# Optimization experiments

Hardware: AMD Instinct MI355X
Metric: run time of the kernel (lower is better)

Reference implementation:

```python
import jax, jax.numpy as jnp
import numpy as np

N, E, G, F, H, L, NH, HD = 40000, 640000, 256, 9, 128, 3, 4, 32
EPS = 1e-5

def _ln(x, g, b):
    m = jnp.mean(x, axis=-1, keepdims=True)
    v = jnp.mean((x - m) ** 2, axis=-1, keepdims=True)
    return (x - m) * jax.lax.rsqrt(v + EPS) * g + b

def _forward(floats, edge_index, batch):
    (x, pos, emb_w, emb_b, edge_w1, edge_b1, edge_w2, edge_b2,
     node_w1, node_b1, node_w2, node_b2, qkv_w, qkv_b, out_w, out_b,
     ln1_g, ln1_b, ln2_g, ln2_b, ff_w1, ff_b1, ff_w2, ff_b2,
     cls_w1, cls_b1, cls_w2, cls_b2) = floats
    src, dst = edge_index[0], edge_index[1]  # PyG: x_j = x[src], x_i = x[dst], aggregate at dst
    dist = jnp.linalg.norm(pos[dst] - pos[src], axis=-1, keepdims=True)  # [E,1]
    h = x @ emb_w + emb_b  # [N,H]
    for l in range(L):
        # message: edge_mlp(cat[x_i, x_j, dist])
        ef = jnp.concatenate([h[dst], h[src], dist], axis=-1)  # [E,2H+1]
        m = jax.nn.silu(ef @ edge_w1[l] + edge_b1[l])
        m = jax.nn.silu(m @ edge_w2[l] + edge_b2[l])  # [E,H]
        aggr = jax.ops.segment_sum(m, dst, num_segments=N)  # [N,H]
        u = jax.nn.silu(jnp.concatenate([h, aggr], axis=-1) @ node_w1[l] + node_b1[l])
        u = u @ node_w2[l] + node_b2[l]
        h = h + u  # residual in GAHT.forward
    # per-graph mean pooling (faithful to masked-mean loop)
    sums = jax.ops.segment_sum(h, batch, num_segments=G)  # [G,H]
    cnts = jax.ops.segment_sum(jnp.ones((N,), h.dtype), batch, num_segments=G)
    g = sums / jnp.maximum(cnts, 1.0)[:, None]  # [G,H]
    # 2-layer post-norm transformer encoder (batch=1, seq=G), relu FFN, eval mode (no dropout)
    scale = 1.0 / jnp.sqrt(jnp.asarray(HD, g.dtype))
    for t in range(2):
        qkv = g @ qkv_w[t] + qkv_b[t]  # [G,3H]
        q, k, v = jnp.split(qkv, 3, axis=-1)
        q = q.reshape(G, NH, HD); k = k.reshape(G, NH, HD); v = v.reshape(G, NH, HD)
        att = jax.nn.softmax(jnp.einsum('qhd,khd->hqk', q, k) * scale, axis=-1)
        o = jnp.einsum('hqk,khd->qhd', att, v).reshape(G, H)
        o = o @ out_w[t] + out_b[t]
        g = _ln(g + o, ln1_g[t], ln1_b[t])
        ff = jax.nn.relu(g @ ff_w1[t] + ff_b1[t]) @ ff_w2[t] + ff_b2[t]
        g = _ln(g + ff, ln2_g[t], ln2_b[t])
    out = jax.nn.relu(g @ cls_w1 + cls_b1) @ cls_w2 + cls_b2  # [G,1]
    return out.squeeze(-1)  # [G]


def setup_inputs() -> dict:
    key = jax.random.key(0)
    ks = jax.random.split(key, 16)
    def p(k, shape, scale=0.08):
        return jax.random.normal(k, shape, dtype=jnp.float32) * scale
    return {
        'x': jax.random.normal(ks[0], (N, F), dtype=jnp.float32),
        'pos': jax.random.normal(ks[1], (N, 3), dtype=jnp.float32),
        'emb_w': p(ks[2], (F, H)), 'emb_b': jnp.zeros((H,), jnp.float32),
        'edge_w1': p(ks[3], (L, 2 * H + 1, H)), 'edge_b1': jnp.zeros((L, H), jnp.float32),
        'edge_w2': p(ks[4], (L, H, H)), 'edge_b2': jnp.zeros((L, H), jnp.float32),
        'node_w1': p(ks[5], (L, 2 * H, H)), 'node_b1': jnp.zeros((L, H), jnp.float32),
        'node_w2': p(ks[6], (L, H, H)), 'node_b2': jnp.zeros((L, H), jnp.float32),
        'qkv_w': p(ks[7], (2, H, 3 * H)), 'qkv_b': jnp.zeros((2, 3 * H), jnp.float32),
        'out_w': p(ks[8], (2, H, H)), 'out_b': jnp.zeros((2, H), jnp.float32),
        'ln1_g': jnp.ones((2, H), jnp.float32), 'ln1_b': jnp.zeros((2, H), jnp.float32),
        'ln2_g': jnp.ones((2, H), jnp.float32), 'ln2_b': jnp.zeros((2, H), jnp.float32),
        'ff_w1': p(ks[9], (2, H, 2 * H)), 'ff_b1': jnp.zeros((2, 2 * H), jnp.float32),
        'ff_w2': p(ks[10], (2, 2 * H, H)), 'ff_b2': jnp.zeros((2, H), jnp.float32),
        'cls_w1': p(ks[11], (H, H // 2)), 'cls_b1': jnp.zeros((H // 2,), jnp.float32),
        'cls_w2': p(ks[12], (H // 2, 1)), 'cls_b2': jnp.zeros((1,), jnp.float32),
        'edge_index': jax.random.randint(ks[13], (2, E), 0, N),
        'batch': jnp.sort(jax.random.randint(ks[14], (N,), 0, G)),
    }


def reference(x, pos, emb_w, emb_b, edge_w1, edge_b1, edge_w2, edge_b2,
              node_w1, node_b1, node_w2, node_b2, qkv_w, qkv_b, out_w, out_b,
              ln1_g, ln1_b, ln2_g, ln2_b, ff_w1, ff_b1, ff_w2, ff_b2,
              cls_w1, cls_b1, cls_w2, cls_b2, edge_index, batch):
    floats = (x, pos, emb_w, emb_b, edge_w1, edge_b1, edge_w2, edge_b2,
              node_w1, node_b1, node_w2, node_b2, qkv_w, qkv_b, out_w, out_b,
              ln1_g, ln1_b, ln2_g, ln2_b, ff_w1, ff_b1, ff_w2, ff_b2,
              cls_w1, cls_b1, cls_w2, cls_b2)
    return _forward(floats, edge_index, batch)
```

## Files before the change

kernel.cpp:

```cpp
#include <hip/hip_runtime.h>
#include <hip/hip_bf16.h>
#include <stdint.h>

#define NN 40000
#define EE 640000
#define GG 256
#define FFE 9
#define HH 128

typedef __bf16 bf16;
typedef __bf16 bf16x8 __attribute__((ext_vector_type(8)));
typedef float f32x4 __attribute__((ext_vector_type(4)));

__device__ __forceinline__ f32x4 mfma16(bf16x8 a, bf16x8 b, f32x4 c){
  return __builtin_amdgcn_mfma_f32_16x16x32_bf16(a, b, c, 0, 0, 0);
}
__device__ __forceinline__ float silu_f(float x){
  return x * __builtin_amdgcn_rcpf(1.0f + __expf(-x));
}
__device__ __forceinline__ uint16_t bfb(float x){ bf16 h=(bf16)x; return *(uint16_t*)&h; }
__device__ __forceinline__ int swz(int row, int cb){
  return row*256 + (cb ^ ((row & 7) << 4));
}

__global__ __launch_bounds__(256) void k_prep(
    const float* __restrict__ edge_w1, const float* __restrict__ edge_w2,
    const float* __restrict__ node_w1, const float* __restrict__ node_w2,
    const float* __restrict__ edge_b1,
    const float* __restrict__ x, const float* __restrict__ emb_w,
    const float* __restrict__ emb_b,
    bf16* __restrict__ wcatT, bf16* __restrict__ w2T,
    bf16* __restrict__ nw1T, bf16* __restrict__ nw2T,
    float* __restrict__ bcat, float* __restrict__ h, bf16* __restrict__ h_bf,
    int* __restrict__ cnt)
{
  int b = blockIdx.x, tid = threadIdx.x;
  if (b < 192){
    int l = b/64; int t2 = (b%64)*256 + tid;
    int n = t2 >> 7, k = t2 & 127;
    wcatT[(size_t)l*32768 + n*128 + k] = (bf16)edge_w1[(size_t)l*32896 + k*128 + n];
  } else if (b < 384){
    int lb = b - 192; int l = lb/64; int t2 = (lb%64)*256 + tid;
    int n = t2 >> 7, k = t2 & 127;
    wcatT[(size_t)l*32768 + 16384 + n*128 + k] = (bf16)edge_w1[(size_t)l*32896 + (128+k)*128 + n];
  } else if (b < 576){
    int lb = b - 384; int l = lb/64; int t2 = (lb%64)*256 + tid;
    int n = t2 >> 7, k = t2 & 127;
    w2T[(size_t)l*16384 + n*128 + k] = (bf16)edge_w2[(size_t)l*16384 + k*128 + n];
  } else if (b < 960){
    int lb = b - 576; int l = lb/128; int t2 = (lb%128)*256 + tid;
    int n = t2 >> 8, k = t2 & 255;
    nw1T[(size_t)l*32768 + n*256 + k] = (bf16)node_w1[(size_t)l*32768 + k*128 + n];
  } else if (b < 1152){
    int lb = b - 960; int l = lb/64; int t2 = (lb%64)*256 + tid;
    int n = t2 >> 7, k = t2 & 127;
    nw2T[(size_t)l*16384 + n*128 + k] = (bf16)node_w2[(size_t)l*16384 + k*128 + n];
  } else if (b < 1155){
    int l = b - 1152;
    bcat[l*256 + tid] = (tid < 128) ? edge_b1[l*128 + tid] : 0.0f;
  } else if (b < 1312){
    int i = (b - 1155)*256 + tid;
    if (i < NN) cnt[i] = 0;
  } else {
    int idx = (b - 1312)*256 + tid;
    int n = idx >> 7, f = idx & 127;
    float s = emb_b[f];
    const float* xr = x + n*FFE;
    #pragma unroll
    for (int k=0;k<FFE;++k) s += xr[k]*emb_w[k*HH + f];
    h[idx] = s;
    h_bf[idx] = (bf16)s;
  }
}

__global__ __launch_bounds__(256) void k_hist(const int* __restrict__ dst, int* __restrict__ cnt){
  int e = blockIdx.x*256 + threadIdx.x;
  if (e < EE) atomicAdd(&cnt[dst[e]], 1);
}

__global__ __launch_bounds__(1024) void k_scan(const int* __restrict__ cnt, int* __restrict__ cursor, int n){
  __shared__ int s_wsum[16];
  __shared__ int s_run;
  int tid = threadIdx.x, lane = tid & 63, wv = tid >> 6;
  if (tid == 0) s_run = 0;
  __syncthreads();
  for (int base=0; base<n; base+=4096){
    int i = base + tid*4;
    int c0 = (i  <n)? cnt[i  ] : 0;
    int c1 = (i+1<n)? cnt[i+1] : 0;
    int c2 = (i+2<n)? cnt[i+2] : 0;
    int c3 = (i+3<n)? cnt[i+3] : 0;
    int t0 = c0, t1 = t0+c1, t2 = t1+c2, t3 = t2+c3;
    int xx = t3;
    #pragma unroll
    for (int off=1; off<64; off<<=1){ int t = __shfl_up(xx, off); if (lane>=off) xx += t; }
    if (lane==63) s_wsum[wv] = xx;
    __syncthreads();
    if (wv==0 && lane<16){
      int y = s_wsum[lane];
      #pragma unroll
      for (int off=1; off<16; off<<=1){ int t = __shfl_up(y, off, 16); if (lane>=off) y += t; }
      s_wsum[lane] = y;
    }
    __syncthreads();
    int woff = wv ? s_wsum[wv-1] : 0;
    int run = s_run;
    int eb = run + woff + xx - t3;
    if (i  <n) cursor[i  ] = eb;
    if (i+1<n) cursor[i+1] = eb + t0;
    if (i+2<n) cursor[i+2] = eb + t1;
    if (i+3<n) cursor[i+3] = eb + t2;
    __syncthreads();
    if (tid==0) s_run = run + s_wsum[15];
    __syncthreads();
  }
}

__global__ __launch_bounds__(256) void k_scatter(
    const int* __restrict__ ei, const float* __restrict__ pos,
    int* __restrict__ cursor, int4* __restrict__ rec)
{
  int e = blockIdx.x*256 + threadIdx.x;
  if (e >= EE) return;
  int s = ei[e], d = ei[EE + e];
  int p = atomicAdd(&cursor[d], 1);
  float dx = pos[d*3+0]-pos[s*3+0];
  float dy = pos[d*3+1]-pos[s*3+1];
  float dz = pos[d*3+2]-pos[s*3+2];
  int4 rc; rc.x = s; rc.y = d; rc.z = __float_as_int(sqrtf(dx*dx+dy*dy+dz*dz)); rc.w = 0;
  rec[p] = rc;
}

template<int KTOT, int K1, int ACT, bool A1BF, bool BIAS, bool RESID, bool OBF, bool OF, bool ZAGGR>
__global__ __launch_bounds__(256) void k_gemm(
    const void* __restrict__ a1v, const float* __restrict__ a2,
    const bf16* __restrict__ wt, const float* __restrict__ bias,
    const float* __restrict__ resid, bf16* __restrict__ outb,
    float* __restrict__ outf, int Nw, float* __restrict__ aggr)
{
  constexpr int LDK = 136;
  __shared__ bf16 s_a[128*LDK];
  __shared__ bf16 s_w[64*LDK];
  int tid = threadIdx.x, lane = tid & 63, w = tid >> 6;
  int m0 = blockIdx.x*128, n0 = blockIdx.y*64;
  if (ZAGGR && blockIdx.y == 0){
    int nrows = NN - m0; if (nrows > 128) nrows = 128;
    f32x4 z = {0.f,0.f,0.f,0.f};
    for (int i = tid; i < nrows*32; i += 256)
      *(f32x4*)(aggr + (size_t)m0*128 + (size_t)i*4) = z;
  }
  f32x4 acc[2][4];
  #pragma unroll
  for (int i=0;i<2;++i)
    #pragma unroll
    for (int j=0;j<4;++j)
      #pragma unroll
      for (int r=0;r<4;++r) acc[i][j][r]=0.f;
  int rsel = lane & 15, ksel = (lane>>4)*8;
  int wm = w*32;

  for (int kh=0; kh<KTOT; kh+=128){
    #pragma unroll
    for (int it=0; it<8; ++it){
      int idx = tid + it*256;
      int row = idx >> 4, col = (idx & 15)*8;
      int gc = kh + col;
      int grow = m0 + row; if (grow > NN-1) grow = NN-1;
      bf16x8 vv;
      if (gc < K1){
        if (A1BF){
          vv = *(const bf16x8*)((const bf16*)a1v + (size_t)grow*K1 + gc);
        } else {
          const float* srcp = (const float*)a1v + (size_t)grow*K1 + gc;
          f32x4 u0 = *(const f32x4*)srcp;
          f32x4 u1 = *(const f32x4*)(srcp+4);
          vv[0]=(bf16)u0[0]; vv[1]=(bf16)u0[1]; vv[2]=(bf16)u0[2]; vv[3]=(bf16)u0[3];
          vv[4]=(bf16)u1[0]; vv[5]=(bf16)u1[1]; vv[6]=(bf16)u1[2]; vv[7]=(bf16)u1[3];
        }
      } else {
        const float* srcp = a2 + (size_t)grow*(KTOT-K1) + (gc-K1);
        f32x4 u0 = *(const f32x4*)srcp;
        f32x4 u1 = *(const f32x4*)(srcp+4);
        vv[0]=(bf16)u0[0]; vv[1]=(bf16)u0[1]; vv[2]=(bf16)u0[2]; vv[3]=(bf16)u0[3];
        vv[4]=(bf16)u1[0]; vv[5]=(bf16)u1[1]; vv[6]=(bf16)u1[2]; vv[7]=(bf16)u1[3];
      }
      *(bf16x8*)&s_a[row*LDK + col] = vv;
    }
    #pragma unroll
    for (int it=0; it<4; ++it){
      int idx = tid + it*256;
      int row = idx >> 4, col = (idx & 15)*8;
      *(bf16x8*)&s_w[row*LDK + col] = *(const bf16x8*)(wt + (size_t)(n0+row)*KTOT + kh + col);
    }
    __syncthreads();
    #pragma unroll
    for (int ks=0; ks<4; ++ks){
      int kb = ks*32 + ksel;
      bf16x8 fa0 = *(const bf16x8*)&s_a[(wm+rsel)*LDK + kb];
      bf16x8 fa1 = *(const bf16x8*)&s_a[(wm+16+rsel)*LDK + kb];
      #pragma unroll
      for (int j=0;j<4;++j){
        bf16x8 fb = *(const bf16x8*)&s_w[(j*16+rsel)*LDK + kb];
        acc[0][j]=mfma16(fa0,fb,acc[0][j]);
        acc[1][j]=mfma16(fa1,fb,acc[1][j]);
      }
    }
    __syncthreads();
  }

  #pragma unroll
  for (int i=0;i<2;++i){
    #pragma unroll
    for (int j=0;j<4;++j){
      int col = n0 + j*16 + rsel;
      float bv = BIAS ? bias[col] : 0.0f;
      #pragma unroll
      for (int r=0;r<4;++r){
        int row = m0 + wm + i*16 + 4*(lane>>4) + r;
        if (row < NN){
          float v = acc[i][j][r] + bv;
          if (ACT==1) v = silu_f(v);
          if (RESID) v += resid[(size_t)row*Nw + col];
          if (OBF) outb[(size_t)row*Nw + col] = (bf16)v;
          if (OF)  outf[(size_t)row*Nw + col] = v;
        }
      }
    }
  }
}

__global__ __launch_bounds__(512, 6) void k_edge(
    const bf16* __restrict__ P, const bf16* __restrict__ w2t,
    const float* __restrict__ w1r, const float* __restrict__ b2,
    const int4* __restrict__ rec, float* __restrict__ aggr)
{
  __shared__ char smem[32768];
  __shared__ int s_dst[128];
  __shared__ unsigned s_segidw[32];
  __shared__ int s_segdst[128];
  __shared__ int s_misc[4];
  int tid = threadIdx.x, lane = tid & 63, w = tid >> 6;
  int rsel = lane & 15, hi = lane >> 4;
  int bid = blockIdx.x;
  int swb = (bid & 7) * (EE/128/8) + (bid >> 3);
  int e0 = swb * 128;
  int col = w*16 + rsel;

  bf16x8 fb[4];
  #pragma unroll
  for (int ks=0;ks<4;++ks)
    fb[ks] = *(const bf16x8*)(w2t + (size_t)col*128 + ks*32 + hi*8);

  if (tid == 0){
    s_misc[0] = (e0 == 0) ? -2147483647 : rec[e0-1].y;
    s_misc[1] = (e0 + 128 >= EE) ? -2147483647 : rec[e0+128].y;
  }

  int cq = (tid & 15)*8;
  int er = tid >> 5;
  er = tid >> 4;
  int4 rc[4];
  #pragma unroll
  for (int it=0; it<4; ++it) rc[it] = rec[e0 + er + it*32];
  uint4 pau[4], pbu[4];
  #pragma unroll
  for (int it=0; it<4; ++it){
    pau[it] = *(const uint4*)(P + ((size_t)rc[it].y << 8) + cq);
    pbu[it] = *(const uint4*)(P + ((size_t)rc[it].x << 8) + 128 + cq);
  }
  if (cq == 0){
    #pragma unroll
    for (int it=0; it<4; ++it) s_dst[er + it*32] = rc[it].y;
  }
  f32x4 wr0 = *(const f32x4*)(w1r + cq);
  f32x4 wr1 = *(const f32x4*)(w1r + cq + 4);
  #pragma unroll
  for (int it=0; it<4; ++it){
    float dist = __int_as_float(rc[it].z);
    bf16x8 mm;
    #pragma unroll
    for (int j=0;j<4;++j){
      unsigned ua = ((const unsigned*)&pau[it])[j];
      unsigned ub = ((const unsigned*)&pbu[it])[j];
      float al = __uint_as_float(ua << 16);
      float ah = __uint_as_float(ua & 0xFFFF0000u);
      float bl = __uint_as_float(ub << 16);
      float bh = __uint_as_float(ub & 0xFFFF0000u);
      float wlo = (j<2) ? wr0[2*j]   : wr1[2*(j-2)];
      float whi = (j<2) ? wr0[2*j+1] : wr1[2*(j-2)+1];
      mm[2*j]   = (bf16)silu_f(al + bl + dist*wlo);
      mm[2*j+1] = (bf16)silu_f(ah + bh + dist*whi);
    }
    *(bf16x8*)(smem + swz(er + it*32, cq*2)) = mm;
  }
  __syncthreads();

  if (w == 0){
    int d0 = s_dst[2*lane], d1 = s_dst[2*lane+1];
    int dm1 = (lane == 0) ? 0 : s_dst[2*lane-1];
    int h0 = (lane == 0) ? 1 : (d0 != dm1);
    int h1 = (d1 != d0);
    int p = h0 + h1, x = p;
    #pragma unroll
    for (int off=1; off<64; off<<=1){ int t = __shfl_up(x, off); if (lane>=off) x += t; }
    int excl = x - p;
    int id0 = excl + h0 - 1;
    int id1 = excl + p - 1;
    uint8_t* sb = (uint8_t*)s_segidw;
    sb[2*lane]   = (uint8_t)id0;
    sb[2*lane+1] = (uint8_t)id1;
    if (h0) s_segdst[id0] = d0;
    if (h1) s_segdst[id1] = d1;
    if (lane == 63) s_misc[2] = id1 + 1;
  }

  f32x4 acc[8];
  #pragma unroll
  for (int mt=0;mt<8;++mt)
    #pragma unroll
    for (int r=0;r<4;++r) acc[mt][r]=0.f;
  #pragma unroll
  for (int mt=0;mt<8;++mt){
    #pragma unroll
    for (int ks=0;ks<4;++ks){
      bf16x8 fa = *(const bf16x8*)(smem + swz(mt*16 + rsel, ks*64 + hi*16));
      acc[mt] = mfma16(fa, fb[ks], acc[mt]);
    }
  }
  __syncthreads();

  float bb = b2[col];
  #pragma unroll
  for (int mt=0;mt<8;++mt){
    uint2 pk;
    pk.x = (unsigned)bfb(silu_f(acc[mt][0] + bb)) | ((unsigned)bfb(silu_f(acc[mt][1] + bb)) << 16);
    pk.y = (unsigned)bfb(silu_f(acc[mt][2] + bb)) | ((unsigned)bfb(silu_f(acc[mt][3] + bb)) << 16);
    *(uint2*)(smem + col*256 + ((mt*32 + hi*8) ^ ((col & 7) << 4))) = pk;
  }
  __syncthreads();

  bf16x8 gb[4];
  #pragma unroll
  for (int ks=0;ks<4;++ks)
    gb[ks] = *(const bf16x8*)(smem + col*256 + ((ks*64 + hi*16) ^ ((col & 7) << 4)));
  int nseg = s_misc[2];
  bool openL = (s_dst[0]   == s_misc[0]);
  bool openR = (s_dst[127] == s_misc[1]);
  for (int st = 0; st < nseg; st += 16){
    unsigned tgt = (unsigned)(st + rsel);
    f32x4 racc = {0.f,0.f,0.f,0.f};
    #pragma unroll
    for (int ks=0;ks<4;++ks){
      unsigned w0 = s_segidw[ks*8 + hi*2];
      unsigned w1 = s_segidw[ks*8 + hi*2 + 1];
      union { uint16_t u[8]; bf16x8 v; } sa;
      #pragma unroll
      for (int j=0;j<4;++j){
        sa.u[j]   = (((w0 >> (8*j)) & 255u) == tgt) ? (uint16_t)0x3F80 : (uint16_t)0;
        sa.u[4+j] = (((w1 >> (8*j)) & 255u) == tgt) ? (uint16_t)0x3F80 : (uint16_t)0;
      }
      racc = mfma16(sa.v, gb[ks], racc);
    }
    #pragma unroll
    for (int r=0;r<4;++r){
      int s = st + 4*hi + r;
      if (s < nseg){
        float v = racc[r];
        size_t off = (size_t)s_segdst[s]*128 + col;
        bool atom = (s == 0 && openL) || (s == nseg-1 && openR);
        if (atom) atomicAdd(&aggr[off], v);
        else      aggr[off] = v;
      }
    }
  }
}

__device__ __forceinline__ int lbound(const int* a, int n, int key){
  int lo=0, hi=n;
  while (lo<hi){ int mid=(lo+hi)>>1; if (a[mid]<key) lo=mid+1; else hi=mid; }
  return lo;
}

__global__ __launch_bounds__(384) void k_pool_qkv(
    const float* __restrict__ h, const int* __restrict__ batch,
    const float* __restrict__ wq, const float* __restrict__ bq,
    float* __restrict__ gbuf, float* __restrict__ qkvb)
{
  __shared__ float sg[128];
  int gr = blockIdx.x, tid = threadIdx.x;
  if (tid < 128){
    int lo = lbound(batch, NN, gr), hi2 = lbound(batch, NN, gr+1);
    float s = 0.f;
    for (int n=lo;n<hi2;++n) s += h[(size_t)n*HH + tid];
    int c = hi2 - lo; if (c < 1) c = 1;
    s /= (float)c;
    sg[tid] = s; gbuf[gr*128 + tid] = s;
  }
  __syncthreads();
  float a = bq[tid];
  for (int k=0;k<128;++k) a += sg[k]*wq[k*384 + tid];
  qkvb[gr*384 + tid] = a;
}

template<int MODE>
__global__ __launch_bounds__(128) void k_tail(
    const float* __restrict__ qkv, const float* __restrict__ wo,
    const float* __restrict__ bo, const float* __restrict__ l1g,
    const float* __restrict__ l1b, const float* __restrict__ w1,
    const float* __restrict__ b1f, const float* __restrict__ w2,
    const float* __restrict__ b2f, const float* __restrict__ l2g,
    const float* __restrict__ l2b, float* __restrict__ gbuf,
    const float* __restrict__ wq2, const float* __restrict__ bq2,
    float* __restrict__ qkvb2,
    const float* __restrict__ cw1, const float* __restrict__ cb1,
    const float* __restrict__ cw2, const float* __restrict__ cb2,
    float* __restrict__ out)
{
  __shared__ float sq[128];
  __shared__ float ss[4][256];
  __shared__ float so[128];
  __shared__ float st[256];
  __shared__ float red[4];
  int r = blockIdx.x, tid = threadIdx.x;
  sq[tid] = qkv[r*384 + tid];
  __syncthreads();
  const float scale = 0.17677669529663687f;
  for (int i=tid; i<1024; i+=128){
    int hh = i >> 8, j = i & 255;
    const float* kr = qkv + j*384 + 128 + hh*32;
    const float* qr = sq + hh*32;
    float s=0;
    #pragma unroll
    for (int d=0;d<32;++d) s += qr[d]*kr[d];
    ss[hh][j] = s*scale;
  }
  __syncthreads();
  int hh = tid >> 5, sl = tid & 31;
  float m = -1e30f;
  #pragma unroll
  for (int q8=0;q8<8;++q8) m = fmaxf(m, ss[hh][sl + q8*32]);
  #pragma unroll
  for (int off=16; off; off>>=1) m = fmaxf(m, __shfl_xor(m, off, 32));
  float sum = 0.f;
  #pragma unroll
  for (int q8=0;q8<8;++q8){
    float e = __expf(ss[hh][sl+q8*32] - m);
    ss[hh][sl+q8*32] = e;
    sum += e;
  }
  #pragma unroll
  for (int off=16; off; off>>=1) sum += __shfl_xor(sum, off, 32);
  float inv = __builtin_amdgcn_rcpf(sum);
  __syncthreads();
  float accv = 0.f;
  for (int j=0;j<256;++j) accv += ss[hh][j]*qkv[j*384 + 256 + hh*32 + sl];
  so[tid] = accv*inv;
  __syncthreads();
  float a = bo[tid];
  for (int k=0;k<128;++k) a += so[k]*wo[k*128 + tid];
  float val = gbuf[r*128 + tid] + a;
  {
    float s = val, q = val*val;
    #pragma unroll
    for (int off=32; off; off>>=1){ s += __shfl_xor(s, off); q += __shfl_xor(q, off); }
    int lane = tid & 63, wv = tid >> 6;
    if (lane==0){ red[wv*2]=s; red[wv*2+1]=q; }
    __syncthreads();
    float S = red[0]+red[2], Q = red[1]+red[3];
    float mean = S*(1.0f/128.0f);
    float var = Q*(1.0f/128.0f) - mean*mean;
    float ninv = rsqrtf(var + 1e-5f);
    val = (val-mean)*ninv*l1g[tid] + l1b[tid];
  }
  sq[tid] = val;
  __syncthreads();
  float a0 = b1f[tid], a1 = b1f[tid+128];
  for (int k=0;k<128;++k){
    float gv = sq[k];
    a0 += gv*w1[k*256 + tid];
    a1 += gv*w1[k*256 + tid + 128];
  }
  st[tid]     = fmaxf(a0, 0.f);
  st[tid+128] = fmaxf(a1, 0.f);
  __syncthreads();
  float b = b2f[tid];
  for (int k=0;k<256;++k) b += st[k]*w2[k*128 + tid];
  float val2 = val + b;
  {
    float s = val2, q = val2*val2;
    #pragma unroll
    for (int off=32; off; off>>=1){ s += __shfl_xor(s, off); q += __shfl_xor(q, off); }
    int lane = tid & 63, wv = tid >> 6;
    __syncthreads();
    if (lane==0){ red[wv*2]=s; red[wv*2+1]=q; }
    __syncthreads();
    float S = red[0]+red[2], Q = red[1]+red[3];
    float mean = S*(1.0f/128.0f);
    float var = Q*(1.0f/128.0f) - mean*mean;
    float ninv = rsqrtf(var + 1e-5f);
    val2 = (val2-mean)*ninv*l2g[tid] + l2b[tid];
  }
  gbuf[r*128 + tid] = val2;
  if (MODE == 0){
    sq[tid] = val2;
    __syncthreads();
    float q0 = bq2[tid], q1 = bq2[tid+128], q2 = bq2[tid+256];
    for (int k=0;k<128;++k){
      float gv = sq[k];
      const float* wr = wq2 + k*384;
      q0 += gv*wr[tid]; q1 += gv*wr[tid+128]; q2 += gv*wr[tid+256];
    }
    qkvb2[r*384+tid]=q0; qkvb2[r*384+tid+128]=q1; qkvb2[r*384+tid+256]=q2;
  }
  if (MODE == 1){
    so[tid] = val2;
    __syncthreads();
    if (tid < 64){
      float c = cb1[tid];
      for (int k=0;k<128;++k) c += so[k]*cw1[k*64 + tid];
      c = fmaxf(c, 0.f);
      float p = c * cw2[tid];
      #pragma unroll
      for (int off=32; off; off>>=1) p += __shfl_xor(p, off);
      if (tid==0) out[r] = p + cb2[0];
    }
  }
}

extern "C" void kernel_launch(void* const* d_in, const int* in_sizes, int n_in,
                              void* d_out, int out_size, void* d_ws, size_t ws_size,
                              hipStream_t stream)
{
  (void)in_sizes; (void)n_in; (void)out_size; (void)ws_size;
  const float* x      = (const float*)d_in[0];
  const float* pos    = (const float*)d_in[1];
  const float* emb_w  = (const float*)d_in[2];
  const float* emb_b  = (const float*)d_in[3];
  const float* edge_w1= (const float*)d_in[4];
  const float* edge_b1= (const float*)d_in[5];
  const float* edge_w2= (const float*)d_in[6];
  const float* edge_b2= (const float*)d_in[7];
  const float* node_w1= (const float*)d_in[8];
  const float* node_b1= (const float*)d_in[9];
  const float* node_w2= (const float*)d_in[10];
  const float* node_b2= (const float*)d_in[11];
  const float* qkv_w  = (const float*)d_in[12];
  const float* qkv_b  = (const float*)d_in[13];
  const float* out_w  = (const float*)d_in[14];
  const float* out_b  = (const float*)d_in[15];
  const float* ln1_g  = (const float*)d_in[16];
  const float* ln1_b  = (const float*)d_in[17];
  const float* ln2_g  = (const float*)d_in[18];
  const float* ln2_b  = (const float*)d_in[19];
  const float* ff_w1  = (const float*)d_in[20];
  const float* ff_b1  = (const float*)d_in[21];
  const float* ff_w2  = (const float*)d_in[22];
  const float* ff_b2  = (const float*)d_in[23];
  const float* cls_w1 = (const float*)d_in[24];
  const float* cls_b1 = (const float*)d_in[25];
  const float* cls_w2 = (const float*)d_in[26];
  const float* cls_b2 = (const float*)d_in[27];
  const int* ei       = (const int*)d_in[28];
  const int* batch    = (const int*)d_in[29];
  float* out = (float*)d_out;

  uint8_t* wp = (uint8_t*)d_ws;
  auto take = [&](size_t nb)->void*{ void* r = wp; wp += (nb + 255) & ~(size_t)255; return r; };
  float* h      = (float*)take((size_t)NN*HH*4);
  bf16*  h_bf   = (bf16*) take((size_t)NN*HH*2);
  bf16*  P      = (bf16*) take((size_t)NN*256*2);
  float* aggr   = (float*)take((size_t)NN*HH*4);
  bf16*  u1     = (bf16*) take((size_t)NN*HH*2);
  int*   cnt    = (int*)  take((size_t)NN*4);
  int*   cursor = (int*)  take((size_t)NN*4);
  int4*  rec    = (int4*) take((size_t)EE*16);
  bf16*  wcatT  = (bf16*) take((size_t)3*256*128*2);
  bf16*  w2T    = (bf16*) take((size_t)3*128*128*2);
  bf16*  nw1T   = (bf16*) take((size_t)3*128*256*2);
  bf16*  nw2T   = (bf16*) take((size_t)3*128*128*2);
  float* bcat   = (float*)take((size_t)3*256*4);
  float* gbuf   = (float*)take((size_t)GG*HH*4);
  float* qkvb   = (float*)take((size_t)GG*384*4);
  float* qkvb2  = (float*)take((size_t)GG*384*4);

  dim3 b256(256);
  k_prep<<<dim3(21312), b256, 0, stream>>>(edge_w1, edge_w2, node_w1, node_w2,
    edge_b1, x, emb_w, emb_b, wcatT, w2T, nw1T, nw2T, bcat, h, h_bf, cnt);
  k_hist<<<dim3(EE/256), b256, 0, stream>>>(ei + EE, cnt);
  k_scan<<<dim3(1), dim3(1024), 0, stream>>>(cnt, cursor, NN);
  k_scatter<<<dim3(EE/256), b256, 0, stream>>>(ei, pos, cursor, rec);

  for (int l=0;l<3;++l){
    k_gemm<128,128,0,true,true,false,true,false,true><<<dim3(313,4), b256, 0, stream>>>(
      h_bf, nullptr, wcatT + (size_t)l*256*128, bcat + (size_t)l*256, nullptr, P, nullptr, 256, aggr);
    k_edge<<<dim3(EE/128), dim3(512), 0, stream>>>(P, w2T + (size_t)l*128*128,
      edge_w1 + ((size_t)l*257 + 256)*128, edge_b2 + (size_t)l*128, rec, aggr);
    k_gemm<256,128,1,true,true,false,true,false,false><<<dim3(313,2), b256, 0, stream>>>(
      h_bf, aggr, nw1T + (size_t)l*128*256, node_b1 + (size_t)l*128, nullptr, u1, nullptr, 128, nullptr);
    k_gemm<128,128,0,true,true,true,true,true,false><<<dim3(313,2), b256, 0, stream>>>(
      u1, nullptr, nw2T + (size_t)l*128*128, node_b2 + (size_t)l*128, h, h_bf, h, 128, nullptr);
  }

  k_pool_qkv<<<dim3(GG), dim3(384), 0, stream>>>(h, batch, qkv_w, qkv_b, gbuf, qkvb);
  k_tail<0><<<dim3(GG), dim3(128), 0, stream>>>(qkvb, out_w, out_b,
    ln1_g, ln1_b, ff_w1, ff_b1, ff_w2, ff_b2, ln2_g, ln2_b, gbuf,
    qkv_w + (size_t)128*384, qkv_b + 384, qkvb2,
    nullptr, nullptr, nullptr, nullptr, nullptr);
  k_tail<1><<<dim3(GG), dim3(128), 0, stream>>>(qkvb2, out_w + (size_t)128*128, out_b + 128,
    ln1_g + 128, ln1_b + 128, ff_w1 + (size_t)128*256, ff_b1 + 256,
    ff_w2 + (size_t)256*128, ff_b2 + 128, ln2_g + 128, ln2_b + 128, gbuf,
    nullptr, nullptr, nullptr,
    cls_w1, cls_b1, cls_w2, cls_b2, out);
}
```

Baseline: 727.1 us.

## Fuse node MLP, residual, and next-layer edge projection into one kernel

```diff
diff --git a/kernel.cpp b/kernel.cpp
--- a/kernel.cpp
+++ b/kernel.cpp
@@ -31,7 +31,7 @@
     const float* __restrict__ emb_b,
     bf16* __restrict__ wcatT, bf16* __restrict__ w2T,
     bf16* __restrict__ nw1T, bf16* __restrict__ nw2T,
-    float* __restrict__ bcat, float* __restrict__ h, bf16* __restrict__ h_bf,
+    float* __restrict__ bcat, float* __restrict__ h,
     int* __restrict__ cnt)
 {
   int b = blockIdx.x, tid = threadIdx.x;
@@ -69,7 +69,6 @@
     #pragma unroll
     for (int k=0;k<FFE;++k) s += xr[k]*emb_w[k*HH + f];
     h[idx] = s;
-    h_bf[idx] = (bf16)s;
   }
 }
 
@@ -229,6 +228,164 @@
   }
 }
 
+template<bool DOP>
+__global__ __launch_bounds__(256) void k_node(
+    float* h, float* aggr,
+    const bf16* __restrict__ nw1t,
+    const bf16* __restrict__ nw2t,
+    const bf16* __restrict__ wct,
+    const float* __restrict__ nb1, const float* __restrict__ nb2,
+    const float* __restrict__ bcv,
+    bf16* __restrict__ P)
+{
+  __shared__ bf16 SA[64][132];
+  __shared__ bf16 SW[128][72];
+  __shared__ bf16 SU[64][132];
+  int tid = threadIdx.x, lane = tid & 63, w = tid >> 6;
+  int rsel = lane & 15, hi = lane >> 4;
+  int m0 = blockIdx.x * 64;
+  int urow = w*16 + rsel;
+  int grow = m0 + urow;
+
+  f32x4 acc[8];
+  #pragma unroll
+  for (int nt=0;nt<8;++nt)
+    #pragma unroll
+    for (int r=0;r<4;++r) acc[nt][r]=0.f;
+
+  for (int kq=0; kq<4; ++kq){
+    const float* src = (kq < 2) ? (h + (size_t)m0*128 + kq*64)
+                                : (aggr + (size_t)m0*128 + (kq-2)*64);
+    #pragma unroll
+    for (int it=0; it<2; ++it){
+      int g = tid + it*256;
+      int row = g >> 3, cg = (g & 7)*8;
+      const float* sp = src + (size_t)row*128 + cg;
+      f32x4 u0 = *(const f32x4*)sp, u1v = *(const f32x4*)(sp+4);
+      bf16x8 vv;
+      vv[0]=(bf16)u0[0]; vv[1]=(bf16)u0[1]; vv[2]=(bf16)u0[2]; vv[3]=(bf16)u0[3];
+      vv[4]=(bf16)u1v[0]; vv[5]=(bf16)u1v[1]; vv[6]=(bf16)u1v[2]; vv[7]=(bf16)u1v[3];
+      *(bf16x8*)&SA[row][cg] = vv;
+    }
+    #pragma unroll
+    for (int it=0; it<4; ++it){
+      int g = tid + it*256;
+      int row = g >> 3, cg = (g & 7)*8;
+      *(bf16x8*)&SW[row][cg] = *(const bf16x8*)(nw1t + (size_t)row*256 + kq*64 + cg);
+    }
+    __syncthreads();
+    #pragma unroll
+    for (int ks=0; ks<2; ++ks){
+      int kb = ks*32 + hi*8;
+      bf16x8 fa = *(const bf16x8*)&SA[w*16 + rsel][kb];
+      #pragma unroll
+      for (int nt=0;nt<8;++nt){
+        bf16x8 fw = *(const bf16x8*)&SW[nt*16 + rsel][kb];
+        acc[nt] = mfma16(fw, fa, acc[nt]);
+      }
+    }
+    __syncthreads();
+  }
+
+  #pragma unroll
+  for (int nt=0;nt<8;++nt){
+    int nb = nt*16 + 4*hi;
+    f32x4 b4 = *(const f32x4*)(nb1 + nb);
+    uint16_t q0 = bfb(silu_f(acc[nt][0] + b4[0]));
+    uint16_t q1 = bfb(silu_f(acc[nt][1] + b4[1]));
+    uint16_t q2 = bfb(silu_f(acc[nt][2] + b4[2]));
+    uint16_t q3 = bfb(silu_f(acc[nt][3] + b4[3]));
+    uint2 pk; pk.x = (unsigned)q0 | ((unsigned)q1 << 16); pk.y = (unsigned)q2 | ((unsigned)q3 << 16);
+    *(uint2*)&SU[urow][nb] = pk;
+  }
+  __syncthreads();
+
+  #pragma unroll
+  for (int nt=0;nt<8;++nt)
+    #pragma unroll
+    for (int r=0;r<4;++r) acc[nt][r]=0.f;
+  for (int kq=0; kq<2; ++kq){
+    #pragma unroll
+    for (int it=0; it<4; ++it){
+      int g = tid + it*256;
+      int row = g >> 3, cg = (g & 7)*8;
+      *(bf16x8*)&SW[row][cg] = *(const bf16x8*)(nw2t + (size_t)row*128 + kq*64 + cg);
+    }
+    __syncthreads();
+    #pragma unroll
+    for (int ks=0; ks<2; ++ks){
+      int kb = ks*32 + hi*8;
+      bf16x8 fa = *(const bf16x8*)&SU[w*16 + rsel][kq*64 + kb];
+      #pragma unroll
+      for (int nt=0;nt<8;++nt){
+        bf16x8 fw = *(const bf16x8*)&SW[nt*16 + rsel][kb];
+        acc[nt] = mfma16(fw, fa, acc[nt]);
+      }
+    }
+    __syncthreads();
+  }
+
+  #pragma unroll
+  for (int nt=0;nt<8;++nt){
+    int nb = nt*16 + 4*hi;
+    f32x4 b4 = *(const f32x4*)(nb2 + nb);
+    f32x4 h4 = *(const f32x4*)(h + (size_t)grow*128 + nb);
+    f32x4 v;
+    #pragma unroll
+    for (int r=0;r<4;++r) v[r] = h4[r] + acc[nt][r] + b4[r];
+    *(f32x4*)(h + (size_t)grow*128 + nb) = v;
+    uint2 pk;
+    pk.x = (unsigned)bfb(v[0]) | ((unsigned)bfb(v[1]) << 16);
+    pk.y = (unsigned)bfb(v[2]) | ((unsigned)bfb(v[3]) << 16);
+    *(uint2*)&SA[urow][nb] = pk;
+  }
+  __syncthreads();
+
+  if (DOP){
+    for (int nh=0; nh<2; ++nh){
+      #pragma unroll
+      for (int nt=0;nt<8;++nt)
+        #pragma unroll
+        for (int r=0;r<4;++r) acc[nt][r]=0.f;
+      for (int kq=0; kq<2; ++kq){
+        #pragma unroll
+        for (int it=0; it<4; ++it){
+          int g = tid + it*256;
+          int row = g >> 3, cg = (g & 7)*8;
+          *(bf16x8*)&SW[row][cg] = *(const bf16x8*)(wct + (size_t)(nh*128+row)*128 + kq*64 + cg);
+        }
+        __syncthreads();
+        #pragma unroll
+        for (int ks=0; ks<2; ++ks){
+          int kb = ks*32 + hi*8;
+          bf16x8 fa = *(const bf16x8*)&SA[w*16 + rsel][kq*64 + kb];
+          #pragma unroll
+          for (int nt=0;nt<8;++nt){
+            bf16x8 fw = *(const bf16x8*)&SW[nt*16 + rsel][kb];
+            acc[nt] = mfma16(fw, fa, acc[nt]);
+          }
+        }
+        __syncthreads();
+      }
+      #pragma unroll
+      for (int nt=0;nt<8;++nt){
+        int nb = nh*128 + nt*16 + 4*hi;
+        f32x4 b4 = *(const f32x4*)(bcv + nb);
+        uint2 pk;
+        pk.x = (unsigned)bfb(acc[nt][0] + b4[0]) | ((unsigned)bfb(acc[nt][1] + b4[1]) << 16);
+        pk.y = (unsigned)bfb(acc[nt][2] + b4[2]) | ((unsigned)bfb(acc[nt][3] + b4[3]) << 16);
+        *(uint2*)(P + (size_t)grow*256 + nb) = pk;
+      }
+    }
+    f32x4 z = {0.f,0.f,0.f,0.f};
+    #pragma unroll
+    for (int it=0; it<8; ++it){
+      int idx = tid + it*256;
+      *(f32x4*)(aggr + (size_t)m0*128 + (size_t)idx*4) = z;
+    }
+  }
+}
+
 __global__ __launch_bounds__(512, 6) void k_edge(
     const bf16* __restrict__ P, const bf16* __restrict__ w2t,
     const float* __restrict__ w1r, const float* __restrict__ b2,
@@ -257,8 +414,7 @@
   }
 
   int cq = (tid & 15)*8;
-  int er = tid >> 5;
-  er = tid >> 4;
+  int er = tid >> 4;
   int4 rc[4];
   #pragma unroll
   for (int it=0; it<4; ++it) rc[it] = rec[e0 + er + it*32];
@@ -567,10 +723,8 @@
   uint8_t* wp = (uint8_t*)d_ws;
   auto take = [&](size_t nb)->void*{ void* r = wp; wp += (nb + 255) & ~(size_t)255; return r; };
   float* h      = (float*)take((size_t)NN*HH*4);
-  bf16*  h_bf   = (bf16*) take((size_t)NN*HH*2);
   bf16*  P      = (bf16*) take((size_t)NN*256*2);
   float* aggr   = (float*)take((size_t)NN*HH*4);
-  bf16*  u1     = (bf16*) take((size_t)NN*HH*2);
   int*   cnt    = (int*)  take((size_t)NN*4);
   int*   cursor = (int*)  take((size_t)NN*4);
   int4*  rec    = (int4*) take((size_t)EE*16);
@@ -585,20 +739,26 @@
 
   dim3 b256(256);
   k_prep<<<dim3(21312), b256, 0, stream>>>(edge_w1, edge_w2, node_w1, node_w2,
-    edge_b1, x, emb_w, emb_b, wcatT, w2T, nw1T, nw2T, bcat, h, h_bf, cnt);
+    edge_b1, x, emb_w, emb_b, wcatT, w2T, nw1T, nw2T, bcat, h, cnt);
   k_hist<<<dim3(EE/256), b256, 0, stream>>>(ei + EE, cnt);
   k_scan<<<dim3(1), dim3(1024), 0, stream>>>(cnt, cursor, NN);
   k_scatter<<<dim3(EE/256), b256, 0, stream>>>(ei, pos, cursor, rec);
 
+  k_gemm<128,128,0,false,true,false,true,false,true><<<dim3(313,4), b256, 0, stream>>>(
+    h, nullptr, wcatT, bcat, nullptr, P, nullptr, 256, aggr);
+
   for (int l=0;l<3;++l){
-    k_gemm<128,128,0,true,true,false,true,false,true><<<dim3(313,4), b256, 0, stream>>>(
-      h_bf, nullptr, wcatT + (size_t)l*256*128, bcat + (size_t)l*256, nullptr, P, nullptr, 256, aggr);
-    k_edge<<<dim3(EE/128), dim3(512), 0, stream>>>(P, w2T + (size_t)l*128*128,
+    k_edge<<<dim3(EE/128), dim3(512), 0, stream>>>(P, w2T + (size_t)l*16384,
       edge_w1 + ((size_t)l*257 + 256)*128, edge_b2 + (size_t)l*128, rec, aggr);
-    k_gemm<256,128,1,true,true,false,true,false,false><<<dim3(313,2), b256, 0, stream>>>(
-      h_bf, aggr, nw1T + (size_t)l*128*256, node_b1 + (size_t)l*128, nullptr, u1, nullptr, 128, nullptr);
-    k_gemm<128,128,0,true,true,true,true,true,false><<<dim3(313,2), b256, 0, stream>>>(
-      u1, nullptr, nw2T + (size_t)l*128*128, node_b2 + (size_t)l*128, h, h_bf, h, 128, nullptr);
+    if (l < 2){
+      k_node<true><<<dim3(625), b256, 0, stream>>>(h, aggr,
+        nw1T + (size_t)l*32768, nw2T + (size_t)l*16384, wcatT + (size_t)(l+1)*32768,
+        node_b1 + (size_t)l*128, node_b2 + (size_t)l*128, bcat + (size_t)(l+1)*256, P);
+    } else {
+      k_node<false><<<dim3(625), b256, 0, stream>>>(h, aggr,
+        nw1T + (size_t)l*32768, nw2T + (size_t)l*16384, wcatT,
+        node_b1 + (size_t)l*128, node_b2 + (size_t)l*128, bcat, P);
+    }
   }
 
   k_pool_qkv<<<dim3(GG), dim3(384), 0, stream>>>(h, batch, qkv_w, qkv_b, gbuf, qkvb);
```

Result: faster. 669.1 us (-8.0%).
